# Kernel tuning notes

Measured on AMD Instinct MI355X. Metric: run time of the kernel, lower is better.

## Reference

```python
import jax, jax.numpy as jnp
import numpy as np

NUM_HEADS = 64
HEAD_DIM = 10  # forced by nn.Linear(10, 1)


def setup_inputs() -> dict:
    key = jax.random.key(0)
    kq, kk, kv, kw = jax.random.split(key, 4)
    B, T, M = 16, 4096, NUM_HEADS * HEAD_DIM
    return {
        "query": jax.random.normal(kq, (B, T, M), dtype=jnp.float32),
        "key": jax.random.normal(kk, (B, T, M), dtype=jnp.float32),
        "value": jax.random.normal(kv, (B, T, M), dtype=jnp.float32),
        "W": jax.random.normal(kw, (1, HEAD_DIM), dtype=jnp.float32) * 0.3,
        "b": jnp.zeros((1,), dtype=jnp.float32),
    }


def _to_heads(x):
    # torch: stack(split(x, head_dim, dim=2), dim=0) -> [H, B, T, D]
    B, T, M = x.shape
    return x.reshape(B, T, NUM_HEADS, HEAD_DIM).transpose(2, 0, 1, 3)


def reference(query, key, value, W, b):
    D = HEAD_DIM
    q = _to_heads(query)   # [H,B,T,D]
    k = _to_heads(key)     # [H,B,T,D]
    v = _to_heads(value)   # [H,B,T,D]
    # key.transpose(-1,-2).sum(3).unsqueeze(2): sum over T -> [H,B,1,D]
    k_sum = k.sum(axis=2, keepdims=True)
    attn = jax.nn.softmax(jnp.tanh(q * k_sum / np.float32(np.sqrt(D))), axis=-1)
    t = attn * v                          # [H,B,T,D]
    v_q = t.sum(axis=2)                   # [H,B,D]
    v_v = t.sum(axis=3).transpose(1, 0, 2)  # [B,H,T]
    # input_proj: Linear(10,1) on v_q*v_q (v_query == v_key == t summed over T)
    s = jnp.tanh((v_q * v_q) @ W.T + b)   # [H,B,1]
    s = jax.nn.softmax(s, axis=-1)        # softmax over size-1 dim (== ones)
    s = s.transpose(1, 0, 2)              # [B,H,1]
    return v_v * s                        # [B,H,T]
```

## Files before the change

kernel.cpp:

```cpp
#include <hip/hip_runtime.h>
#include <stdint.h>

#define BB 16
#define TT 4096
#define HH 64
#define MM 640

#define TROWS 16
#define PADF4 41

__global__ void __launch_bounds__(256)
ksum_kernel(const float* __restrict__ key, float* __restrict__ ksum) {
    int g = blockIdx.x * blockDim.x + threadIdx.x;
    int b = g / 160;
    int c = g % 160;
    int t0 = blockIdx.y * 32;

    const float4* p = reinterpret_cast<const float4*>(key)
                    + (size_t)b * TT * 160 + (size_t)t0 * 160 + c;

    float4 a0 = make_float4(0.f,0.f,0.f,0.f);
    float4 a1 = make_float4(0.f,0.f,0.f,0.f);
    float4 a2 = make_float4(0.f,0.f,0.f,0.f);
    float4 a3 = make_float4(0.f,0.f,0.f,0.f);
    #pragma unroll
    for (int i = 0; i < 32; i += 4) {
        float4 x0 = p[(size_t)(i + 0) * 160];
        float4 x1 = p[(size_t)(i + 1) * 160];
        float4 x2 = p[(size_t)(i + 2) * 160];
        float4 x3 = p[(size_t)(i + 3) * 160];
        a0.x += x0.x; a0.y += x0.y; a0.z += x0.z; a0.w += x0.w;
        a1.x += x1.x; a1.y += x1.y; a1.z += x1.z; a1.w += x1.w;
        a2.x += x2.x; a2.y += x2.y; a2.z += x2.z; a2.w += x2.w;
        a3.x += x3.x; a3.y += x3.y; a3.z += x3.z; a3.w += x3.w;
    }
    float sx = (a0.x + a1.x) + (a2.x + a3.x);
    float sy = (a0.y + a1.y) + (a2.y + a3.y);
    float sz = (a0.z + a1.z) + (a2.z + a3.z);
    float sw = (a0.w + a1.w) + (a2.w + a3.w);

    float* dst = ksum + b * MM + c * 4;
    atomicAdd(dst + 0, sx);
    atomicAdd(dst + 1, sy);
    atomicAdd(dst + 2, sz);
    atomicAdd(dst + 3, sw);
}

__device__ __forceinline__ float tanh_rcp(float x) {
    float ax = fabsf(x);
    float e2 = __expf(-2.0f * ax);
    float th = (1.0f - e2) * __builtin_amdgcn_rcpf(1.0f + e2);
    return copysignf(th, x);
}

__global__ void __launch_bounds__(128)
attn_kernel(const float* __restrict__ q,
            const float* __restrict__ v,
            const float* __restrict__ ksum,
            float* __restrict__ out) {
    __shared__ float qs[TROWS * PADF4 * 4];
    __shared__ float vs[TROWS * PADF4 * 4];
    __shared__ float ks_lds[160];

    const int tid = threadIdx.x;
    const int t0  = blockIdx.x * TROWS;
    const int hg  = blockIdx.y;
    const int b   = blockIdx.z;

    const float4* qg = reinterpret_cast<const float4*>(q)
                     + ((size_t)(b * TT + t0)) * 160 + hg * 40;
    const float4* vg = reinterpret_cast<const float4*>(v)
                     + ((size_t)(b * TT + t0)) * 160 + hg * 40;

    float4 rq[5], rv[5];
    #pragma unroll
    for (int j = 0; j < 5; ++j) {
        int idx = tid + 128 * j;
        int row = idx / 40;
        int c   = idx % 40;
        rq[j] = qg[(size_t)row * 160 + c];
        rv[j] = vg[(size_t)row * 160 + c];
    }
    if (tid < 40) {
        reinterpret_cast<float4*>(ks_lds)[tid] =
            reinterpret_cast<const float4*>(ksum + b * MM + hg * 160)[tid];
    }

    float4* qs4 = reinterpret_cast<float4*>(qs);
    float4* vs4 = reinterpret_cast<float4*>(vs);
    #pragma unroll
    for (int j = 0; j < 5; ++j) {
        int idx = tid + 128 * j;
        int row = idx / 40;
        int c   = idx % 40;
        qs4[row * PADF4 + c] = rq[j];
        vs4[row * PADF4 + c] = rv[j];
    }
    __syncthreads();

    const float R = 0.316227766016838f;
    const int head0 = tid >> 4;
    const int row   = tid & 15;

    float ksr0[10], ksr1[10];
    #pragma unroll
    for (int d = 0; d < 10; ++d) {
        ksr0[d] = ks_lds[head0 * 10 + d] * R;
        ksr1[d] = ks_lds[(head0 + 8) * 10 + d] * R;
    }

    #pragma unroll
    for (int o = 0; o < 2; ++o) {
        const int head  = head0 + o * 8;
        const int lbase = row * (PADF4 * 4) + head * 10;
        const float* kk = o ? ksr1 : ksr0;
        float sum = 0.f, dot = 0.f;
        #pragma unroll
        for (int d = 0; d < 10; ++d) {
            float e = __expf(tanh_rcp(qs[lbase + d] * kk[d]));
            sum += e;
            dot += e * vs[lbase + d];
        }
        out[((size_t)(b * HH + hg * 16 + head)) * TT + t0 + row]
            = dot * __builtin_amdgcn_rcpf(sum);
    }
}

extern "C" void kernel_launch(void* const* d_in, const int* in_sizes, int n_in,
                              void* d_out, int out_size, void* d_ws, size_t ws_size,
                              hipStream_t stream) {
    const float* q = (const float*)d_in[0];
    const float* k = (const float*)d_in[1];
    const float* v = (const float*)d_in[2];
    float* out  = (float*)d_out;
    float* ksum = (float*)d_ws;

    hipMemsetAsync(d_ws, 0, (size_t)BB * MM * sizeof(float), stream);
    ksum_kernel<<<dim3(10, 128), dim3(256), 0, stream>>>(k, ksum);
    attn_kernel<<<dim3(TT / TROWS, 4, BB), dim3(128), 0, stream>>>(q, v, ksum, out);
}
```

Baseline: 112.9 us.

## Make attn kernel single-wavefront persistent blocks looping over row tiles

The attention kernel now launches 4096 blocks of one 64-thread wavefront, each looping over 8 tiles of 8 rows, instead of 16384 blocks of 128 threads handling 16 rows once. The ksum values are loaded into registers once per block and reused across tiles. Because a block is a single wavefront, the __syncthreads between the LDS staging stores and the reads is dropped, and LDS reads use float2. The intent is to cut block launch and synchronisation overhead and amortise the ksum setup, at the cost of serialising the load and compute phases inside each block with no overlap. The LDS tile is also reused across iterations with no barrier, which depends on in-order execution within a single wavefront.

```diff
diff --git a/kernel.cpp b/kernel.cpp
--- a/kernel.cpp
+++ b/kernel.cpp
@@ -6,8 +6,8 @@
 #define HH 64
 #define MM 640
 
-#define TROWS 16
 #define PADF4 41
+#define ROWSF (PADF4 * 4)
 
 __global__ void __launch_bounds__(256)
 ksum_kernel(const float* __restrict__ key, float* __restrict__ ksum) {
@@ -53,76 +53,90 @@
     return copysignf(th, x);
 }
 
-__global__ void __launch_bounds__(128)
+__global__ void __launch_bounds__(64)
 attn_kernel(const float* __restrict__ q,
             const float* __restrict__ v,
             const float* __restrict__ ksum,
             float* __restrict__ out) {
-    __shared__ float qs[TROWS * PADF4 * 4];
-    __shared__ float vs[TROWS * PADF4 * 4];
+    __shared__ float qs[8 * ROWSF];
+    __shared__ float vs[8 * ROWSF];
     __shared__ float ks_lds[160];
 
-    const int tid = threadIdx.x;
-    const int t0  = blockIdx.x * TROWS;
-    const int hg  = blockIdx.y;
-    const int b   = blockIdx.z;
+    const int lane = threadIdx.x;
+    const int bid  = blockIdx.x;
+    const int part = bid & 63;
+    const int hg   = (bid >> 6) & 3;
+    const int b    = bid >> 8;
 
-    const float4* qg = reinterpret_cast<const float4*>(q)
-                     + ((size_t)(b * TT + t0)) * 160 + hg * 40;
-    const float4* vg = reinterpret_cast<const float4*>(v)
-                     + ((size_t)(b * TT + t0)) * 160 + hg * 40;
+    if (lane < 40) {
+        reinterpret_cast<float4*>(ks_lds)[lane] =
+            reinterpret_cast<const float4*>(ksum + b * MM + hg * 160)[lane];
+    }
 
-    float4 rq[5], rv[5];
+    const int row = lane & 7;
+    const int hq  = lane >> 3;
+
+    int srow[5], scol[5];
     #pragma unroll
     for (int j = 0; j < 5; ++j) {
-        int idx = tid + 128 * j;
-        int row = idx / 40;
-        int c   = idx % 40;
-        rq[j] = qg[(size_t)row * 160 + c];
-        rv[j] = vg[(size_t)row * 160 + c];
+        int s = lane + 64 * j;
+        srow[j] = s / 40;
+        scol[j] = s % 40;
     }
-    if (tid < 40) {
-        reinterpret_cast<float4*>(ks_lds)[tid] =
-            reinterpret_cast<const float4*>(ksum + b * MM + hg * 160)[tid];
-    }
+
+    const float R = 0.316227766016838f;
+    float ksr[2][10];
+    #pragma unroll
+    for (int o = 0; o < 2; ++o)
+        #pragma unroll
+        for (int d = 0; d < 10; ++d)
+            ksr[o][d] = ks_lds[(hq + 8 * o) * 10 + d] * R;
+
+    const float4* qg0 = reinterpret_cast<const float4*>(q)
+                      + (size_t)b * TT * 160 + hg * 40;
+    const float4* vg0 = reinterpret_cast<const float4*>(v)
+                      + (size_t)b * TT * 160 + hg * 40;
+    float* ob0 = out + ((size_t)(b * HH + hg * 16 + hq)) * TT;
 
     float4* qs4 = reinterpret_cast<float4*>(qs);
     float4* vs4 = reinterpret_cast<float4*>(vs);
-    #pragma unroll
-    for (int j = 0; j < 5; ++j) {
-        int idx = tid + 128 * j;
-        int row = idx / 40;
-        int c   = idx % 40;
-        qs4[row * PADF4 + c] = rq[j];
-        vs4[row * PADF4 + c] = rv[j];
-    }
-    __syncthreads();
 
-    const float R = 0.316227766016838f;
-    const int head0 = tid >> 4;
-    const int row   = tid & 15;
+    #pragma unroll 1
+    for (int i = 0; i < 8; ++i) {
+        const int t0 = part * 64 + i * 8;
 
-    float ksr0[10], ksr1[10];
-    #pragma unroll
-    for (int d = 0; d < 10; ++d) {
-        ksr0[d] = ks_lds[head0 * 10 + d] * R;
-        ksr1[d] = ks_lds[(head0 + 8) * 10 + d] * R;
-    }
+        const float4* qg = qg0 + (size_t)t0 * 160;
+        const float4* vg = vg0 + (size_t)t0 * 160;
+        float4 rq[5], rv[5];
+        #pragma unroll
+        for (int j = 0; j < 5; ++j) {
+            rq[j] = qg[srow[j] * 160 + scol[j]];
+            rv[j] = vg[srow[j] * 160 + scol[j]];
+        }
+        #pragma unroll
+        for (int j = 0; j < 5; ++j) {
+            qs4[srow[j] * PADF4 + scol[j]] = rq[j];
+            vs4[srow[j] * PADF4 + scol[j]] = rv[j];
+        }
 
-    #pragma unroll
-    for (int o = 0; o < 2; ++o) {
-        const int head  = head0 + o * 8;
-        const int lbase = row * (PADF4 * 4) + head * 10;
-        const float* kk = o ? ksr1 : ksr0;
-        float sum = 0.f, dot = 0.f;
         #pragma unroll
-        for (int d = 0; d < 10; ++d) {
-            float e = __expf(tanh_rcp(qs[lbase + d] * kk[d]));
-            sum += e;
-            dot += e * vs[lbase + d];
+        for (int o = 0; o < 2; ++o) {
+            const int fb = row * ROWSF + (hq + 8 * o) * 10;
+            const float2* qp2 = reinterpret_cast<const float2*>(qs + fb);
+            const float2* vp2 = reinterpret_cast<const float2*>(vs + fb);
+            float sum = 0.f, dot = 0.f;
+            #pragma unroll
+            for (int p = 0; p < 5; ++p) {
+                float2 qq = qp2[p];
+                float2 vv = vp2[p];
+                float e0 = __expf(tanh_rcp(qq.x * ksr[o][2*p]));
+                float e1 = __expf(tanh_rcp(qq.y * ksr[o][2*p+1]));
+                sum += e0 + e1;
+                dot += e0 * vv.x + e1 * vv.y;
+            }
+            ob0[(size_t)(8 * o) * TT + t0 + row]
+                = dot * __builtin_amdgcn_rcpf(sum);
         }
-        out[((size_t)(b * HH + hg * 16 + head)) * TT + t0 + row]
-            = dot * __builtin_amdgcn_rcpf(sum);
     }
 }
 
@@ -137,5 +151,5 @@
 
     hipMemsetAsync(d_ws, 0, (size_t)BB * MM * sizeof(float), stream);
     ksum_kernel<<<dim3(10, 128), dim3(256), 0, stream>>>(k, ksum);
-    attn_kernel<<<dim3(TT / TROWS, 4, BB), dim3(128), 0, stream>>>(q, v, ksum, out);
+    attn_kernel<<<dim3(4096), dim3(64), 0, stream>>>(q, v, ksum, out);
 }
```

Result: slower. 129.6 us (+14.8%).
